# Optimization experiments

Hardware: AMD Instinct MI355X
Metric: run time of the kernel (lower is better)

Reference implementation:

```python
import jax, jax.numpy as jnp
import numpy as np

MAX_FLOW = 80.0
STEPS = 200
STEP_SIZE = 10.0
EPS = 1e-5
NOISE_STD = 0.05
GRAD_CLIP = 0.03


def _energy(flow, img1, img2, log_weights):
    # flow: (B,2,H,W), img1/img2: (B,3,H,W); returns per-sample energy (B,)
    _, _, H, W = img1.shape
    flow = flow * MAX_FLOW
    img1 = (img1 + 1.0) / 2.0
    img2 = (img2 + 1.0) / 2.0
    A = jnp.sum((img1 - img2) ** 2, axis=1)                       # (B,H,W)
    data_term = jnp.sum(jnp.sqrt(A + EPS), axis=(1, 2))           # (B,)
    # kernel_dx/_dy are per-channel [-1,1] finite differences -> slicing
    dx = flow[:, :, :, 1:] - flow[:, :, :, :-1]                   # (B,2,H,W-1)
    dy = flow[:, :, 1:, :] - flow[:, :, :-1, :]                   # (B,2,H-1,W)
    Bx = jnp.pad(jnp.sum(dx ** 2, axis=1), ((0, 0), (0, 0), (0, 1)))
    By = jnp.pad(jnp.sum(dy ** 2, axis=1), ((0, 0), (0, 1), (0, 0)))
    smooth_term = jnp.sum(jnp.sqrt(Bx + By + EPS), axis=(1, 2))   # (B,)
    out = jnp.exp(log_weights[0]) * data_term + jnp.exp(log_weights[1]) * smooth_term
    return out / (H * W)


def _langevin_sample(init, img2, log_weights, key):
    # 200-step Langevin MCMC: noise inject, clamp, energy grad, clipped update, clamp
    def energy_sum(x):
        flow, img1 = x[:, :2], x[:, 2:]
        return jnp.sum(_energy(flow, img1, img2, log_weights))

    grad_fn = jax.grad(energy_sum)

    def step(x, k):
        noise = NOISE_STD * jax.random.normal(k, x.shape, x.dtype)
        x = jnp.clip(x + noise, -1.0, 1.0)
        g = jnp.clip(grad_fn(x), -GRAD_CLIP, GRAD_CLIP)
        x = jnp.clip(x - STEP_SIZE * g, -1.0, 1.0)
        return x, None

    keys = jax.random.split(key, STEPS)
    x, _ = jax.lax.scan(step, init, keys)
    return x


def setup_inputs() -> dict:
    key = jax.random.key(0)
    k1, k2, k3, k4 = jax.random.split(key, 4)
    B, H, W = 8, 384, 512
    target1 = jax.random.normal(k1, (B, 2, H, W), dtype=jnp.float32)
    input1 = jax.random.uniform(k2, (B, 3, H, W), dtype=jnp.float32)
    input2 = jax.random.uniform(k3, (B, 3, H, W), dtype=jnp.float32)
    init = jax.random.uniform(k4, (B, 5, H, W), dtype=jnp.float32) * 2.0 - 1.0
    log_weights = jnp.ones((2,), dtype=jnp.float32)
    return {"target1": target1, "input1": input1, "input2": input2,
            "init": init, "log_weights": log_weights}


def reference(target1, input1, input2, init, log_weights):
    flow_pos = target1 / MAX_FLOW
    img1_pos = input1 * 2.0 - 1.0
    img2 = input2 * 2.0 - 1.0
    # negative samples via Langevin MCMC; detached as in the torch module
    neg = jax.lax.stop_gradient(_langevin_sample(init, img2, log_weights, jax.random.key(1)))
    flow_neg, img1_neg = neg[:, :2], neg[:, 2:]
    pos_energy = _energy(flow_pos, img1_pos, img2, log_weights)
    neg_energy = _energy(flow_neg, img1_neg, img2, log_weights)
    energies = jnp.stack([pos_energy, neg_energy])  # (2,B)
    return energies, flow_neg * MAX_FLOW, (img1_neg + 1.0) / 2.0
```

## Files before the change

kernel.cpp:

```cpp
#include <hip/hip_runtime.h>
#include <math.h>

#define HH 384
#define WW 512
#define HW 196608
#define HHW 98304
#define CHW 983040
#define NTOT 7864320
#define FLOW_N 3145728
#define OUT_FLOW_OFF 16
#define OUT_IMG_OFF (16 + FLOW_N)
#define EPS_F 1e-5f
#define EPS_S (1e-5f / 6400.0f)
#define INV_HW (1.0f/196608.0f)

__device__ __forceinline__ float rsq_f(float x)  { return __builtin_amdgcn_rsqf(x); }
__device__ __forceinline__ float ln_f(float x)   { return 0.69314718055994531f * __builtin_amdgcn_logf(x); }
__device__ __forceinline__ float sqrt_f(float x) { return __builtin_amdgcn_sqrtf(x); }

__host__ __device__ __forceinline__ void tf2x32(unsigned k0, unsigned k1,
                                                unsigned x0, unsigned x1,
                                                unsigned& o0, unsigned& o1) {
  const unsigned ks2 = k0 ^ k1 ^ 0x1BD11BDAu;
  x0 += k0; x1 += k1;
#define TFR(r) x0 += x1; x1 = (x1 << (r)) | (x1 >> (32 - (r))); x1 ^= x0;
  TFR(13) TFR(15) TFR(26) TFR(6)
  x0 += k1;  x1 += ks2 + 1u;
  TFR(17) TFR(29) TFR(16) TFR(24)
  x0 += ks2; x1 += k0 + 2u;
  TFR(13) TFR(15) TFR(26) TFR(6)
  x0 += k0;  x1 += k1 + 3u;
  TFR(17) TFR(29) TFR(16) TFR(24)
  x0 += k1;  x1 += ks2 + 4u;
  TFR(13) TFR(15) TFR(26) TFR(6)
  x0 += ks2; x1 += k0 + 5u;
#undef TFR
  o0 = x0; o1 = x1;
}

__device__ __forceinline__ float noise_from_bits(unsigned bits) {
  const float LO = -0.99999994f;
  float f = __uint_as_float((bits >> 9) | 0x3F800000u) - 1.0f;
  float u = fmaxf(LO, f * 2.0f + LO);
  float w = -ln_f((1.0f - u) * (1.0f + u));
  float p;
  if (w < 5.0f) {
    w -= 2.5f;
    p = 2.81022636e-08f;
    p = p * w + 3.43273939e-07f;
    p = p * w + -3.5233877e-06f;
    p = p * w + -4.39150654e-06f;
    p = p * w + 0.00021858087f;
    p = p * w + -0.00125372503f;
    p = p * w + -0.00417768164f;
    p = p * w + 0.246640727f;
    p = p * w + 1.50140941f;
  } else {
    w = sqrt_f(w) - 3.0f;
    p = -0.000200214257f;
    p = p * w + 0.000100950558f;
    p = p * w + 0.00134934322f;
    p = p * w + -0.00367342844f;
    p = p * w + 0.00573950773f;
    p = p * w + -0.0076224613f;
    p = p * w + 0.00943887047f;
    p = p * w + 1.00167406f;
    p = p * w + 2.83297682f;
  }
  float z = 1.4142135623730951f * (p * u);
  return 0.05f * z;
}

__device__ __forceinline__ float upd(float x, float g) {
  g = fminf(fmaxf(g, -0.03f), 0.03f);
  return fminf(fmaxf(x - 10.0f * g, -1.0f), 1.0f);
}

__device__ __forceinline__ float noise_at(unsigned ka, unsigned kb, unsigned idx) {
  unsigned o0, o1;
  tf2x32(ka, kb, 0u, idx, o0, o1);
  return noise_from_bits(o0 ^ o1);
}

__device__ __forceinline__ void noise_store2(float* dst, const float xn[2],
                                             unsigned ka, unsigned kb, unsigned idx0) {
  float r0 = fminf(fmaxf(xn[0] + noise_at(ka, kb, idx0), -1.0f), 1.0f);
  float r1 = fminf(fmaxf(xn[1] + noise_at(ka, kb, idx0 + 1u), -1.0f), 1.0f);
  *(float2*)dst = make_float2(r0, r1);
}

__global__ void k_init(double* acc, float* sw, const float* lw) {
  int t = threadIdx.x;
  if (t < 32) acc[t] = 0.0;
  if (t == 32) {
    sw[0] = expf(lw[0]) * INV_HW * 0.5f;
    sw[1] = expf(lw[1]) * INV_HW * 80.0f;
  }
}

__global__ __launch_bounds__(256) void k_fnoise0(const float* __restrict__ init,
    float* __restrict__ Y, unsigned ka, unsigned kb) {
  int e = blockIdx.x * 256 + threadIdx.x;
  int b = e / (2 * HW);
  int r = e - b * 2 * HW;
  int orig = b * CHW + r;
  float nz = noise_at(ka, kb, (unsigned)orig);
  Y[e] = fminf(fmaxf(init[orig] + nz, -1.0f), 1.0f);
}

template <bool FINAL>
__global__ __launch_bounds__(256, 8) void k_fstep(const float* __restrict__ X,
    float* __restrict__ Y, const float* __restrict__ sw,
    unsigned ka, unsigned kb) {
  int tid = blockIdx.x * 256 + threadIdx.x;
  int b = tid / HHW;
  int q = tid - b * HHW;
  int p = q * 2;
  int h = p >> 9, w = p & 511;
  float s1 = sw[1];
  const float* F0 = X + b * 2 * HW;
  const float* F1 = F0 + HW;
  const bool wpos = (w > 0), wend = (w == 510);
  const bool hpos = (h > 0), hlast = (h == 383);

  float cf[2][3], fm1[2], dw[2][2], dwm1[2], uf[2][3];
  {
    float2 a0 = *(const float2*)(F0 + p);
    float2 a1 = *(const float2*)(F1 + p);
    cf[0][0] = a0.x; cf[0][1] = a0.y;
    cf[1][0] = a1.x; cf[1][1] = a1.y;
    cf[0][2] = wend ? cf[0][1] : F0[p + 2];
    cf[1][2] = wend ? cf[1][1] : F1[p + 2];
    fm1[0] = wpos ? F0[p - 1] : cf[0][0];
    fm1[1] = wpos ? F1[p - 1] : cf[1][0];
    if (!hlast) {
      float2 d0 = *(const float2*)(F0 + p + WW);
      float2 d1 = *(const float2*)(F1 + p + WW);
      dw[0][0] = d0.x; dw[0][1] = d0.y;
      dw[1][0] = d1.x; dw[1][1] = d1.y;
      dwm1[0] = wpos ? F0[p + WW - 1] : fm1[0];
      dwm1[1] = wpos ? F1[p + WW - 1] : fm1[1];
    } else {
#pragma unroll
      for (int c = 0; c < 2; ++c) {
        dw[c][0] = cf[c][0]; dw[c][1] = cf[c][1];
        dwm1[c] = fm1[c];
      }
    }
    if (hpos) {
      float2 u0 = *(const float2*)(F0 + p - WW);
      float2 u1 = *(const float2*)(F1 + p - WW);
      uf[0][0] = u0.x; uf[0][1] = u0.y;
      uf[1][0] = u1.x; uf[1][1] = u1.y;
      uf[0][2] = wend ? uf[0][1] : F0[p - WW + 2];
      uf[1][2] = wend ? uf[1][1] : F1[p - WW + 2];
    } else {
#pragma unroll
      for (int c = 0; c < 2; ++c)
        for (int j = 0; j < 3; ++j) uf[c][j] = cf[c][j];
    }
  }

  float dxc[2][2], dyc[2][2], invSc[2], dxu[2][2], dyu[2][2], invSu[2];
  float dxl[2], dyl[2], invSL;
#pragma unroll
  for (int j = 0; j < 2; ++j) {
#pragma unroll
    for (int c = 0; c < 2; ++c) {
      dxc[c][j] = cf[c][j + 1] - cf[c][j];
      dyc[c][j] = dw[c][j] - cf[c][j];
      dxu[c][j] = uf[c][j + 1] - uf[c][j];
      dyu[c][j] = cf[c][j] - uf[c][j];
    }
    invSc[j] = rsq_f(dxc[0][j]*dxc[0][j] + dxc[1][j]*dxc[1][j]
                   + dyc[0][j]*dyc[0][j] + dyc[1][j]*dyc[1][j] + EPS_S);
    invSu[j] = rsq_f(dxu[0][j]*dxu[0][j] + dxu[1][j]*dxu[1][j]
                   + dyu[0][j]*dyu[0][j] + dyu[1][j]*dyu[1][j] + EPS_S);
  }
  dxl[0] = cf[0][0] - fm1[0];  dxl[1] = cf[1][0] - fm1[1];
  dyl[0] = dwm1[0] - fm1[0];   dyl[1] = dwm1[1] - fm1[1];
  invSL = rsq_f(dxl[0]*dxl[0] + dxl[1]*dxl[1]
              + dyl[0]*dyl[0] + dyl[1]*dyl[1] + EPS_S);

  float xnF[2][2];
#pragma unroll
  for (int j = 0; j < 2; ++j) {
#pragma unroll
    for (int c = 0; c < 2; ++c) {
      float g = -(dxc[c][j] + dyc[c][j]) * invSc[j];
      if (j == 0) { if (wpos) g += dxl[c] * invSL; }
      else        { g += dxc[c][0] * invSc[0]; }
      if (hpos)   { g += dyu[c][j] * invSu[j]; }
      xnF[c][j] = upd(cf[c][j], g * s1);
    }
  }

  if (!FINAL) {
    int nbase = b * CHW + p;
    int sb = b * 2 * HW + p;
    noise_store2(Y + sb,      xnF[0], ka, kb, (unsigned)nbase);
    noise_store2(Y + sb + HW, xnF[1], ka, kb, (unsigned)(nbase + HW));
  } else {
    float* outF = Y + OUT_FLOW_OFF + b * 2 * HW;
    *(float2*)(outF + p)      = make_float2(xnF[0][0]*80.f, xnF[0][1]*80.f);
    *(float2*)(outF + HW + p) = make_float2(xnF[1][0]*80.f, xnF[1][1]*80.f);
  }
}

__global__ __launch_bounds__(256, 8) void k_img(const float* __restrict__ init,
    const float* __restrict__ in2, const float* __restrict__ sw,
    float* __restrict__ out) {
  __shared__ unsigned Kl[400];
  int tid = threadIdx.x;
  if (tid < 200) {
    unsigned a, bb;
    tf2x32(0u, 1u, 0u, (unsigned)tid, a, bb);
    Kl[2 * tid] = a; Kl[2 * tid + 1] = bb;
  }
  __syncthreads();
  int g = blockIdx.x * 256 + tid;
  int b = g / HW;
  int p = g - b * HW;
  float s0 = sw[0];
  unsigned base = (unsigned)(b * CHW + 2 * HW + p);
  float x0 = init[base], x1 = init[base + HW], x2 = init[base + 2 * HW];
  const float* I2 = in2 + b * 3 * HW + p;
  float i0 = ((I2[0] * 2.0f - 1.0f) + 1.0f) * 0.5f;
  float i1 = ((I2[HW] * 2.0f - 1.0f) + 1.0f) * 0.5f;
  float i2v = ((I2[2 * HW] * 2.0f - 1.0f) + 1.0f) * 0.5f;

  for (int t = 0; t < 200; ++t) {
    unsigned ka = Kl[2 * t], kb = Kl[2 * t + 1];
    x0 = fminf(fmaxf(x0 + noise_at(ka, kb, base), -1.0f), 1.0f);
    x1 = fminf(fmaxf(x1 + noise_at(ka, kb, base + HW), -1.0f), 1.0f);
    x2 = fminf(fmaxf(x2 + noise_at(ka, kb, base + 2 * HW), -1.0f), 1.0f);
    float d0 = (x0 + 1.0f) * 0.5f - i0;
    float d1 = (x1 + 1.0f) * 0.5f - i1;
    float d2 = (x2 + 1.0f) * 0.5f - i2v;
    float A = d0*d0 + d1*d1 + d2*d2;
    float sI = s0 * rsq_f(A + EPS_F);
    x0 = upd(x0, d0 * sI);
    x1 = upd(x1, d1 * sI);
    x2 = upd(x2, d2 * sI);
  }
  float* outI = out + OUT_IMG_OFF + b * 3 * HW + p;
  outI[0]      = (x0 + 1.0f) * 0.5f;
  outI[HW]     = (x1 + 1.0f) * 0.5f;
  outI[2 * HW] = (x2 + 1.0f) * 0.5f;
}

__device__ __forceinline__ void block_acc2(double v0, double v1, double* a0, double* a1) {
  for (int off = 32; off > 0; off >>= 1) {
    v0 += __shfl_down(v0, off, 64);
    v1 += __shfl_down(v1, off, 64);
  }
  __shared__ double s0m[4], s1m[4];
  int lane = threadIdx.x & 63, wv = threadIdx.x >> 6;
  if (lane == 0) { s0m[wv] = v0; s1m[wv] = v1; }
  __syncthreads();
  if (threadIdx.x == 0) {
    atomicAdd(a0, s0m[0] + s0m[1] + s0m[2] + s0m[3]);
    atomicAdd(a1, s1m[0] + s1m[1] + s1m[2] + s1m[3]);
  }
}

__global__ __launch_bounds__(256) void k_pos_energy(const float* __restrict__ t1,
    const float* __restrict__ in1, const float* __restrict__ in2,
    double* __restrict__ acc) {
  int blk = blockIdx.x;
  int b = blk / 96;
  int local = blk - b * 96;
  const float* T0 = t1 + b * 2 * HW;
  const float* T1 = T0 + HW;
  const float* I1 = in1 + b * 3 * HW;
  const float* I2 = in2 + b * 3 * HW;
  double data = 0.0, smooth = 0.0;
  for (int it = 0; it < 8; ++it) {
    int p = (local * 8 + it) * 256 + threadIdx.x;
    int h = p >> 9, w = p & 511;
    float f00 = (T0[p] / 80.0f) * 80.0f;
    float f10 = (T1[p] / 80.0f) * 80.0f;
    float dx0 = 0, dx1 = 0, dy0 = 0, dy1 = 0;
    if (w < 511) { dx0 = (T0[p+1]/80.0f)*80.0f - f00;  dx1 = (T1[p+1]/80.0f)*80.0f - f10; }
    if (h < 383) { dy0 = (T0[p+WW]/80.0f)*80.0f - f00; dy1 = (T1[p+WW]/80.0f)*80.0f - f10; }
    smooth += (double)sqrtf(dx0*dx0 + dx1*dx1 + dy0*dy0 + dy1*dy1 + EPS_F);
    float d0 = ((I1[p]*2.0f-1.0f)+1.0f)*0.5f        - ((I2[p]*2.0f-1.0f)+1.0f)*0.5f;
    float d1 = ((I1[p+HW]*2.0f-1.0f)+1.0f)*0.5f     - ((I2[p+HW]*2.0f-1.0f)+1.0f)*0.5f;
    float d2 = ((I1[p+2*HW]*2.0f-1.0f)+1.0f)*0.5f   - ((I2[p+2*HW]*2.0f-1.0f)+1.0f)*0.5f;
    data += (double)sqrtf(d0*d0 + d1*d1 + d2*d2 + EPS_F);
  }
  block_acc2(data, smooth, &acc[b], &acc[8 + b]);
}

__global__ __launch_bounds__(256) void k_neg_energy(const float* __restrict__ out,
    const float* __restrict__ in2, double* __restrict__ acc) {
  int blk = blockIdx.x;
  int b = blk / 96;
  int local = blk - b * 96;
  const float* F0 = out + OUT_FLOW_OFF + b * 2 * HW;
  const float* F1 = F0 + HW;
  const float* I = out + OUT_IMG_OFF + b * 3 * HW;
  const float* I2 = in2 + b * 3 * HW;
  double data = 0.0, smooth = 0.0;
  for (int it = 0; it < 8; ++it) {
    int p = (local * 8 + it) * 256 + threadIdx.x;
    int h = p >> 9, w = p & 511;
    float f00 = F0[p], f10 = F1[p];
    float dx0 = 0, dx1 = 0, dy0 = 0, dy1 = 0;
    if (w < 511) { dx0 = F0[p + 1] - f00;  dx1 = F1[p + 1] - f10; }
    if (h < 383) { dy0 = F0[p + WW] - f00; dy1 = F1[p + WW] - f10; }
    smooth += (double)sqrtf(dx0*dx0 + dx1*dx1 + dy0*dy0 + dy1*dy1 + EPS_F);
    float d0 = I[p]        - ((I2[p]*2.0f-1.0f)+1.0f)*0.5f;
    float d1 = I[p+HW]     - ((I2[p+HW]*2.0f-1.0f)+1.0f)*0.5f;
    float d2 = I[p+2*HW]   - ((I2[p+2*HW]*2.0f-1.0f)+1.0f)*0.5f;
    data += (double)sqrtf(d0*d0 + d1*d1 + d2*d2 + EPS_F);
  }
  block_acc2(data, smooth, &acc[16 + b], &acc[24 + b]);
}

__global__ void k_finalize(const double* __restrict__ acc,
                           const float* __restrict__ lw, float* __restrict__ out) {
  int t = threadIdx.x;
  if (t < 16) {
    int b = t & 7, neg = t >> 3;
    double data   = acc[neg * 16 + b];
    double smooth = acc[neg * 16 + 8 + b];
    double e0 = exp((double)lw[0]), e1 = exp((double)lw[1]);
    out[t] = (float)((e0 * data + e1 * smooth) / 196608.0);
  }
}

extern "C" void kernel_launch(void* const* d_in, const int* in_sizes, int n_in,
                              void* d_out, int out_size, void* d_ws, size_t ws_size,
                              hipStream_t stream) {
  const float* t1  = (const float*)d_in[0];
  const float* in1 = (const float*)d_in[1];
  const float* in2 = (const float*)d_in[2];
  const float* init = (const float*)d_in[3];
  const float* lw  = (const float*)d_in[4];
  float* out = (float*)d_out;

  double* acc = (double*)d_ws;
  float* sw = (float*)((char*)d_ws + 256);
  float* bufFA = (float*)((char*)d_ws + 2048);
  size_t need = 2048 + 2 * (size_t)FLOW_N * sizeof(float);
  float* bufFB = (ws_size >= need) ? bufFA + FLOW_N
                                   : out + OUT_FLOW_OFF;

  unsigned K0[200], K1[200];
  for (int t = 0; t < 200; ++t) tf2x32(0u, 1u, 0u, (unsigned)t, K0[t], K1[t]);

  k_init<<<1, 64, 0, stream>>>(acc, sw, lw);
  k_pos_energy<<<8 * 96, 256, 0, stream>>>(t1, in1, in2, acc);

  k_fnoise0<<<FLOW_N / 256, 256, 0, stream>>>(init, bufFB, K0[0], K1[0]);
  for (int t = 0; t < 199; ++t) {
    const float* src = (t % 2 == 0) ? bufFB : bufFA;
    float* dst       = (t % 2 == 0) ? bufFA : bufFB;
    k_fstep<false><<<8 * HHW / 256, 256, 0, stream>>>(src, dst, sw,
                                                      K0[t + 1], K1[t + 1]);
  }
  k_fstep<true><<<8 * HHW / 256, 256, 0, stream>>>(bufFA, out, sw, 0u, 0u);

  k_img<<<8 * HW / 256, 256, 0, stream>>>(init, in2, sw, out);

  k_neg_energy<<<8 * 96, 256, 0, stream>>>(out, in2, acc);
  k_finalize<<<1, 64, 0, stream>>>(acc, lw, out);
}
```

Measured before the change: 5.322 ms.

## Fuse two Langevin flow steps per kernel using shared-memory halo tiles

Replaces the one-step-per-launch flow update with a temporally blocked kernel. Each block loads a 36x36 tile with a two-pixel clamped halo into LDS. It computes the intermediate step on a 34x34 region, adds noise, and then computes the second step on the 32x32 interior. This halves the number of launches and the global memory round trips across the 200 steps. The cost is redundant halo computation and RNG work, plus synchronisation and LDS use per block. The image-channel loop also prefetches the next step's key from LDS.

```diff
diff --git a/kernel.cpp b/kernel.cpp
--- a/kernel.cpp
+++ b/kernel.cpp
@@ -4,7 +4,6 @@
 #define HH 384
 #define WW 512
 #define HW 196608
-#define HHW 98304
 #define CHW 983040
 #define NTOT 7864320
 #define FLOW_N 3145728
@@ -82,11 +81,8 @@
   return noise_from_bits(o0 ^ o1);
 }
 
-__device__ __forceinline__ void noise_store2(float* dst, const float xn[2],
-                                             unsigned ka, unsigned kb, unsigned idx0) {
-  float r0 = fminf(fmaxf(xn[0] + noise_at(ka, kb, idx0), -1.0f), 1.0f);
-  float r1 = fminf(fmaxf(xn[1] + noise_at(ka, kb, idx0 + 1u), -1.0f), 1.0f);
-  *(float2*)dst = make_float2(r0, r1);
+__device__ __forceinline__ float clip1(float x) {
+  return fminf(fmaxf(x, -1.0f), 1.0f);
 }
 
 __global__ void k_init(double* acc, float* sw, const float* lw) {
@@ -105,114 +101,125 @@
   int r = e - b * 2 * HW;
   int orig = b * CHW + r;
   float nz = noise_at(ka, kb, (unsigned)orig);
-  Y[e] = fminf(fmaxf(init[orig] + nz, -1.0f), 1.0f);
+  Y[e] = clip1(init[orig] + nz);
 }
 
 template <bool FINAL>
-__global__ __launch_bounds__(256, 8) void k_fstep(const float* __restrict__ X,
+__global__ __launch_bounds__(256) void k_f2(const float* __restrict__ X,
     float* __restrict__ Y, const float* __restrict__ sw,
-    unsigned ka, unsigned kb) {
-  int tid = blockIdx.x * 256 + threadIdx.x;
-  int b = tid / HHW;
-  int q = tid - b * HHW;
-  int p = q * 2;
-  int h = p >> 9, w = p & 511;
-  float s1 = sw[1];
-  const float* F0 = X + b * 2 * HW;
-  const float* F1 = F0 + HW;
-  const bool wpos = (w > 0), wend = (w == 510);
-  const bool hpos = (h > 0), hlast = (h == 383);
-
-  float cf[2][3], fm1[2], dw[2][2], dwm1[2], uf[2][3];
-  {
-    float2 a0 = *(const float2*)(F0 + p);
-    float2 a1 = *(const float2*)(F1 + p);
-    cf[0][0] = a0.x; cf[0][1] = a0.y;
-    cf[1][0] = a1.x; cf[1][1] = a1.y;
-    cf[0][2] = wend ? cf[0][1] : F0[p + 2];
-    cf[1][2] = wend ? cf[1][1] : F1[p + 2];
-    fm1[0] = wpos ? F0[p - 1] : cf[0][0];
-    fm1[1] = wpos ? F1[p - 1] : cf[1][0];
-    if (!hlast) {
-      float2 d0 = *(const float2*)(F0 + p + WW);
-      float2 d1 = *(const float2*)(F1 + p + WW);
-      dw[0][0] = d0.x; dw[0][1] = d0.y;
-      dw[1][0] = d1.x; dw[1][1] = d1.y;
-      dwm1[0] = wpos ? F0[p + WW - 1] : fm1[0];
-      dwm1[1] = wpos ? F1[p + WW - 1] : fm1[1];
+    unsigned kA0, unsigned kA1, unsigned kB0, unsigned kB1) {
+  __shared__ float S0[2][36 * 36];
+  __shared__ float S1[2][34 * 34];
+  const int tid = threadIdx.x;
+  const int bid = blockIdx.x;
+  const int b  = bid / 192;
+  const int rr = bid - b * 192;
+  const int h0 = (rr / 16) * 32;
+  const int w0 = (rr & 15) * 32;
+  const float s1v = sw[1];
+  const float* Fb = X + b * 2 * HW;
+
+#pragma unroll
+  for (int ch = 0; ch < 2; ++ch) {
+    const float* F = Fb + ch * HW;
+    for (int idx = tid; idx < 1296; idx += 256) {
+      int i = idx / 36, j = idx - i * 36;
+      int gh = min(max(h0 + i - 2, 0), 383);
+      int gw = min(max(w0 + j - 2, 0), 511);
+      S0[ch][idx] = F[gh * 512 + gw];
+    }
+  }
+  __syncthreads();
+
+  for (int r = tid; r < 1156; r += 256) {
+    int i = r / 34, j = r - i * 34;
+    int c00 = (i + 1) * 36 + (j + 1);
+    float C0 = S0[0][c00],      C1 = S0[1][c00];
+    float R0 = S0[0][c00 + 1],  R1 = S0[1][c00 + 1];
+    float L0 = S0[0][c00 - 1],  L1 = S0[1][c00 - 1];
+    float D0 = S0[0][c00 + 36], D1 = S0[1][c00 + 36];
+    float U0 = S0[0][c00 - 36], U1 = S0[1][c00 - 36];
+    float DL0 = S0[0][c00 + 35], DL1 = S0[1][c00 + 35];
+    float UR0 = S0[0][c00 - 35], UR1 = S0[1][c00 - 35];
+    float dxc0 = R0 - C0, dxc1 = R1 - C1;
+    float dyc0 = D0 - C0, dyc1 = D1 - C1;
+    float invSc = rsq_f(dxc0*dxc0 + dxc1*dxc1 + dyc0*dyc0 + dyc1*dyc1 + EPS_S);
+    float dxl0 = C0 - L0, dxl1 = C1 - L1;
+    float dyl0 = DL0 - L0, dyl1 = DL1 - L1;
+    float invSL = rsq_f(dxl0*dxl0 + dxl1*dxl1 + dyl0*dyl0 + dyl1*dyl1 + EPS_S);
+    float dxu0 = UR0 - U0, dxu1 = UR1 - U1;
+    float dyu0 = C0 - U0, dyu1 = C1 - U1;
+    float invSu = rsq_f(dxu0*dxu0 + dxu1*dxu1 + dyu0*dyu0 + dyu1*dyu1 + EPS_S);
+    float g0 = -(dxc0 + dyc0) * invSc;
+    g0 += dxl0 * invSL;
+    g0 += dyu0 * invSu;
+    float g1 = -(dxc1 + dyc1) * invSc;
+    g1 += dxl1 * invSL;
+    g1 += dyu1 * invSu;
+    float x0 = upd(C0, g0 * s1v);
+    float x1 = upd(C1, g1 * s1v);
+    int gh = h0 + i - 1, gw = w0 + j - 1;
+    unsigned nidx = (unsigned)(b * CHW + gh * 512 + gw);
+    S1[0][r] = clip1(x0 + noise_at(kA0, kA1, nidx));
+    S1[1][r] = clip1(x1 + noise_at(kA0, kA1, nidx + (unsigned)HW));
+  }
+  __syncthreads();
+
+  for (int r = tid; r < 1024; r += 256) {
+    int i = r >> 5, j = r & 31;
+    int gh = h0 + i, gw = w0 + j;
+    int ii = i + 1, jj = j + 1;
+    int iu = (gh > 0)   ? ii - 1 : ii;
+    int id = (gh < 383) ? ii + 1 : ii;
+    int jl = (gw > 0)   ? jj - 1 : jj;
+    int jr = (gw < 511) ? jj + 1 : jj;
+    int cC = ii * 34 + jj;
+    int cR = ii * 34 + jr, cL = ii * 34 + jl;
+    int cD = id * 34 + jj, cU = iu * 34 + jj;
+    int cDL = id * 34 + jl, cUR = iu * 34 + jr;
+    float C0 = S1[0][cC],  C1 = S1[1][cC];
+    float R0 = S1[0][cR],  R1 = S1[1][cR];
+    float L0 = S1[0][cL],  L1 = S1[1][cL];
+    float D0 = S1[0][cD],  D1 = S1[1][cD];
+    float U0 = S1[0][cU],  U1 = S1[1][cU];
+    float DL0 = S1[0][cDL], DL1 = S1[1][cDL];
+    float UR0 = S1[0][cUR], UR1 = S1[1][cUR];
+    float dxc0 = R0 - C0, dxc1 = R1 - C1;
+    float dyc0 = D0 - C0, dyc1 = D1 - C1;
+    float invSc = rsq_f(dxc0*dxc0 + dxc1*dxc1 + dyc0*dyc0 + dyc1*dyc1 + EPS_S);
+    float dxl0 = C0 - L0, dxl1 = C1 - L1;
+    float dyl0 = DL0 - L0, dyl1 = DL1 - L1;
+    float invSL = rsq_f(dxl0*dxl0 + dxl1*dxl1 + dyl0*dyl0 + dyl1*dyl1 + EPS_S);
+    float dxu0 = UR0 - U0, dxu1 = UR1 - U1;
+    float dyu0 = C0 - U0, dyu1 = C1 - U1;
+    float invSu = rsq_f(dxu0*dxu0 + dxu1*dxu1 + dyu0*dyu0 + dyu1*dyu1 + EPS_S);
+    float g0 = -(dxc0 + dyc0) * invSc;
+    g0 += dxl0 * invSL;
+    g0 += dyu0 * invSu;
+    float g1 = -(dxc1 + dyc1) * invSc;
+    g1 += dxl1 * invSL;
+    g1 += dyu1 * invSu;
+    float x0 = upd(C0, g0 * s1v);
+    float x1 = upd(C1, g1 * s1v);
+    int off = gh * 512 + gw;
+    if (!FINAL) {
+      unsigned nidx = (unsigned)(b * CHW + off);
+      Y[b * 2 * HW + off]      = clip1(x0 + noise_at(kB0, kB1, nidx));
+      Y[b * 2 * HW + HW + off] = clip1(x1 + noise_at(kB0, kB1, nidx + (unsigned)HW));
     } else {
-#pragma unroll
-      for (int c = 0; c < 2; ++c) {
-        dw[c][0] = cf[c][0]; dw[c][1] = cf[c][1];
-        dwm1[c] = fm1[c];
-      }
+      float* outF = Y + OUT_FLOW_OFF + b * 2 * HW;
+      outF[off]      = x0 * 80.0f;
+      outF[HW + off] = x1 * 80.0f;
     }
-    if (hpos) {
-      float2 u0 = *(const float2*)(F0 + p - WW);
-      float2 u1 = *(const float2*)(F1 + p - WW);
-      uf[0][0] = u0.x; uf[0][1] = u0.y;
-      uf[1][0] = u1.x; uf[1][1] = u1.y;
-      uf[0][2] = wend ? uf[0][1] : F0[p - WW + 2];
-      uf[1][2] = wend ? uf[1][1] : F1[p - WW + 2];
-    } else {
-#pragma unroll
-      for (int c = 0; c < 2; ++c)
-        for (int j = 0; j < 3; ++j) uf[c][j] = cf[c][j];
-    }
-  }
-
-  float dxc[2][2], dyc[2][2], invSc[2], dxu[2][2], dyu[2][2], invSu[2];
-  float dxl[2], dyl[2], invSL;
-#pragma unroll
-  for (int j = 0; j < 2; ++j) {
-#pragma unroll
-    for (int c = 0; c < 2; ++c) {
-      dxc[c][j] = cf[c][j + 1] - cf[c][j];
-      dyc[c][j] = dw[c][j] - cf[c][j];
-      dxu[c][j] = uf[c][j + 1] - uf[c][j];
-      dyu[c][j] = cf[c][j] - uf[c][j];
-    }
-    invSc[j] = rsq_f(dxc[0][j]*dxc[0][j] + dxc[1][j]*dxc[1][j]
-                   + dyc[0][j]*dyc[0][j] + dyc[1][j]*dyc[1][j] + EPS_S);
-    invSu[j] = rsq_f(dxu[0][j]*dxu[0][j] + dxu[1][j]*dxu[1][j]
-                   + dyu[0][j]*dyu[0][j] + dyu[1][j]*dyu[1][j] + EPS_S);
-  }
-  dxl[0] = cf[0][0] - fm1[0];  dxl[1] = cf[1][0] - fm1[1];
-  dyl[0] = dwm1[0] - fm1[0];   dyl[1] = dwm1[1] - fm1[1];
-  invSL = rsq_f(dxl[0]*dxl[0] + dxl[1]*dxl[1]
-              + dyl[0]*dyl[0] + dyl[1]*dyl[1] + EPS_S);
-
-  float xnF[2][2];
-#pragma unroll
-  for (int j = 0; j < 2; ++j) {
-#pragma unroll
-    for (int c = 0; c < 2; ++c) {
-      float g = -(dxc[c][j] + dyc[c][j]) * invSc[j];
-      if (j == 0) { if (wpos) g += dxl[c] * invSL; }
-      else        { g += dxc[c][0] * invSc[0]; }
-      if (hpos)   { g += dyu[c][j] * invSu[j]; }
-      xnF[c][j] = upd(cf[c][j], g * s1);
-    }
-  }
-
-  if (!FINAL) {
-    int nbase = b * CHW + p;
-    int sb = b * 2 * HW + p;
-    noise_store2(Y + sb,      xnF[0], ka, kb, (unsigned)nbase);
-    noise_store2(Y + sb + HW, xnF[1], ka, kb, (unsigned)(nbase + HW));
-  } else {
-    float* outF = Y + OUT_FLOW_OFF + b * 2 * HW;
-    *(float2*)(outF + p)      = make_float2(xnF[0][0]*80.f, xnF[0][1]*80.f);
-    *(float2*)(outF + HW + p) = make_float2(xnF[1][0]*80.f, xnF[1][1]*80.f);
   }
 }
 
 __global__ __launch_bounds__(256, 8) void k_img(const float* __restrict__ init,
     const float* __restrict__ in2, const float* __restrict__ sw,
     float* __restrict__ out) {
-  __shared__ unsigned Kl[400];
+  __shared__ unsigned Kl[404];
   int tid = threadIdx.x;
-  if (tid < 200) {
+  if (tid < 202) {
     unsigned a, bb;
     tf2x32(0u, 1u, 0u, (unsigned)tid, a, bb);
     Kl[2 * tid] = a; Kl[2 * tid + 1] = bb;
@@ -229,11 +236,12 @@
   float i1 = ((I2[HW] * 2.0f - 1.0f) + 1.0f) * 0.5f;
   float i2v = ((I2[2 * HW] * 2.0f - 1.0f) + 1.0f) * 0.5f;
 
+  unsigned ka = Kl[0], kb = Kl[1];
   for (int t = 0; t < 200; ++t) {
-    unsigned ka = Kl[2 * t], kb = Kl[2 * t + 1];
-    x0 = fminf(fmaxf(x0 + noise_at(ka, kb, base), -1.0f), 1.0f);
-    x1 = fminf(fmaxf(x1 + noise_at(ka, kb, base + HW), -1.0f), 1.0f);
-    x2 = fminf(fmaxf(x2 + noise_at(ka, kb, base + 2 * HW), -1.0f), 1.0f);
+    unsigned kan = Kl[2 * t + 2], kbn = Kl[2 * t + 3];
+    x0 = clip1(x0 + noise_at(ka, kb, base));
+    x1 = clip1(x1 + noise_at(ka, kb, base + HW));
+    x2 = clip1(x2 + noise_at(ka, kb, base + 2 * HW));
     float d0 = (x0 + 1.0f) * 0.5f - i0;
     float d1 = (x1 + 1.0f) * 0.5f - i1;
     float d2 = (x2 + 1.0f) * 0.5f - i2v;
@@ -242,6 +250,7 @@
     x0 = upd(x0, d0 * sI);
     x1 = upd(x1, d1 * sI);
     x2 = upd(x2, d2 * sI);
+    ka = kan; kb = kbn;
   }
   float* outI = out + OUT_IMG_OFF + b * 3 * HW + p;
   outI[0]      = (x0 + 1.0f) * 0.5f;
@@ -354,13 +363,14 @@
   k_pos_energy<<<8 * 96, 256, 0, stream>>>(t1, in1, in2, acc);
 
   k_fnoise0<<<FLOW_N / 256, 256, 0, stream>>>(init, bufFB, K0[0], K1[0]);
-  for (int t = 0; t < 199; ++t) {
-    const float* src = (t % 2 == 0) ? bufFB : bufFA;
-    float* dst       = (t % 2 == 0) ? bufFA : bufFB;
-    k_fstep<false><<<8 * HHW / 256, 256, 0, stream>>>(src, dst, sw,
-                                                      K0[t + 1], K1[t + 1]);
-  }
-  k_fstep<true><<<8 * HHW / 256, 256, 0, stream>>>(bufFA, out, sw, 0u, 0u);
+  for (int j = 0; j < 99; ++j) {
+    const float* src = (j % 2 == 0) ? bufFB : bufFA;
+    float* dst       = (j % 2 == 0) ? bufFA : bufFB;
+    k_f2<false><<<1536, 256, 0, stream>>>(src, dst, sw,
+                                          K0[2*j+1], K1[2*j+1],
+                                          K0[2*j+2], K1[2*j+2]);
+  }
+  k_f2<true><<<1536, 256, 0, stream>>>(bufFA, out, sw, K0[199], K1[199], 0u, 0u);
 
   k_img<<<8 * HW / 256, 256, 0, stream>>>(init, in2, sw, out);
 
```

After: 5.265 ms. About the same (-1.1%).
